# Kernel optimization log

Measured on AMD Instinct MI355X. Metric: run time of the kernel, lower is better.

The kernel has to match this reference:

```python
import jax, jax.numpy as jnp
import numpy as np


def _conv1x1(x, W, b):
    # x: (B, Ci, H, W), W: (Co, Ci), b: (Co,)
    return jnp.einsum('oi,bihw->bohw', W, x) + b[None, :, None, None]


def setup_inputs() -> dict:
    key = jax.random.key(0)
    ks = jax.random.split(key, 12)
    B, C, H, W = 4, 256, 64, 64
    d = C // 2
    prev_c = 512
    s = lambda k, shape, scale=0.05: (jax.random.normal(k, shape, dtype=jnp.float32) * scale)
    return {
        'source_enc_f': jax.random.normal(ks[0], (B, C, H, W), dtype=jnp.float32),
        'target_enc_f': jax.random.normal(ks[1], (B, C, H, W), dtype=jnp.float32),
        'prev_inp': jax.random.normal(ks[2], (B, prev_c, H // 2, W // 2), dtype=jnp.float32),
        'Wq': s(ks[3], (d, C)), 'bq': s(ks[4], (d,)),
        'Wk': s(ks[5], (d, C)), 'bk': s(ks[6], (d,)),
        'Wv': s(ks[7], (d, C)), 'bv': s(ks[8], (d,)),
        'Wp': s(ks[9], (C, d)), 'bp': s(ks[10], (C,)),
        'gamma': jnp.zeros((1,), dtype=jnp.float32) + 0.1,  # nonzero so attn path contributes
        'Wc': s(ks[11], (C, C + prev_c, 3, 3)),
        'bc': jnp.zeros((C,), dtype=jnp.float32),
    }


def reference(source_enc_f, target_enc_f, prev_inp, Wq, bq, Wk, bk, Wv, bv, Wp, bp, gamma, Wc, bc):
    B, C, H, W = source_enc_f.shape
    d = Wq.shape[0]
    HW = H * W

    # --- AttnMech ---
    q = _conv1x1(source_enc_f, Wq, bq)   # (B, d, H, W)
    k = _conv1x1(target_enc_f, Wk, bk)
    v = _conv1x1(target_enc_f, Wv, bv)

    kf = k.reshape(B, d, HW)             # (B, d, HW)
    qf = q.reshape(B, d, HW)             # (B, d, HW)
    # scores[b, i, j] = sum_c key[b, c, i] * query[b, c, j]; no 1/sqrt(d) scaling
    scores = jnp.einsum('bci,bcj->bij', kf, qf)       # (B, HW, HW)
    attn = jax.nn.softmax(scores, axis=1)             # softmax over key axis (torch dim=1)

    vf = v.transpose(0, 2, 3, 1).reshape(B, HW, d)    # (B, HW, d)
    out = jnp.einsum('bij,bjc->bic', attn, vf)        # (B, HW, d)
    out = out.reshape(B, H, W, d).transpose(0, 3, 1, 2)  # (B, d, H, W)
    out = _conv1x1(out, Wp, bp)                       # (B, C, H, W)
    x = target_enc_f + gamma[0] * out

    # --- upsample (nearest, scale 2) + concat ---
    prev = jnp.repeat(jnp.repeat(prev_inp, 2, axis=2), 2, axis=3)
    x = jnp.concatenate([x, prev], axis=1)            # (B, C+prev_c, H, W)

    # --- 3x3 conv, stride 1, pad 1 ---
    x = jax.lax.conv_general_dilated(
        x, Wc, window_strides=(1, 1), padding=((1, 1), (1, 1)),
        dimension_numbers=('NCHW', 'OIHW', 'NCHW'))
    x = x + bc[None, :, None, None]

    # --- InstanceNorm2d (affine=False, eps=1e-5, biased var over HW) ---
    mean = jnp.mean(x, axis=(2, 3), keepdims=True)
    var = jnp.mean(jnp.square(x - mean), axis=(2, 3), keepdims=True)
    x = (x - mean) * jax.lax.rsqrt(var + 1e-5)

    return jax.nn.relu(x)
```

## Files before the change

### kernel.cpp

```cpp
#include <hip/hip_runtime.h>
#include <hip/hip_bf16.h>

#define BB 4
#define CC 256
#define HW 4096
#define DD 128

typedef __attribute__((ext_vector_type(8))) short bf16x8;
typedef __attribute__((ext_vector_type(4))) short bf16x4;
typedef __attribute__((ext_vector_type(4))) float f32x4;
typedef __attribute__((ext_vector_type(16))) float f32x16;
typedef __attribute__((ext_vector_type(4))) unsigned uint4v;

static __device__ __forceinline__ void ld4(float* dst, const float* src) {
  float4 t = *(const float4*)src;
  dst[0] = t.x; dst[1] = t.y; dst[2] = t.z; dst[3] = t.w;
}

static __device__ __forceinline__ short f2b(float f) {
  unsigned u = __float_as_uint(f);
  u += 0x7fffu + ((u >> 16) & 1u);
  return (short)(u >> 16);
}
static __device__ __forceinline__ unsigned pk2(float lo, float hi) {
  return (unsigned)(unsigned short)f2b(lo) | ((unsigned)(unsigned short)f2b(hi) << 16);
}

static __device__ __forceinline__ void gl16(const short* g, short* l) {
  __builtin_amdgcn_global_load_lds(
      (const __attribute__((address_space(1))) unsigned*)g,
      (__attribute__((address_space(3))) unsigned*)l, 16, 0, 0);
}

__global__ __launch_bounds__(256) void k_qkv_mfma(
    const float* __restrict__ src, const float* __restrict__ tgt,
    const float* __restrict__ Wq, const float* __restrict__ bq,
    const float* __restrict__ Wk, const float* __restrict__ bk,
    const float* __restrict__ Wv, const float* __restrict__ bv,
    short* __restrict__ qb, short* __restrict__ kb, short* __restrict__ vb)
{
  __shared__ __align__(16) short Wt[128 * 40];
  __shared__ __align__(16) short Xt[64 * 40];
  __shared__ __align__(16) short T[9216];
  const int tid = threadIdx.x;
  const int wv = tid >> 6;
  const int lane = tid & 63;
  const int t = lane & 15, q = lane >> 4;
  const int px0 = blockIdx.x * 64;
  const int which = blockIdx.y;
  const int b = blockIdx.z;
  const float* X    = (which == 0) ? src : tgt;
  const float* Wm   = (which == 0) ? Wq : (which == 1) ? Wk : Wv;
  const float* bias = (which == 0) ? bq : (which == 1) ? bk : bv;

  const f32x4 zf = {0.f, 0.f, 0.f, 0.f};
  f32x4 acc[2][4];
#pragma unroll
  for (int mt = 0; mt < 2; ++mt)
#pragma unroll
    for (int nt = 0; nt < 4; ++nt) acc[mt][nt] = zf;

  for (int kk = 0; kk < CC; kk += 32) {
    __syncthreads();
#pragma unroll
    for (int u = 0; u < 4; ++u) {
      int e = tid + (u << 8);
      int row = e >> 3, cq = (e & 7) * 4;
      float4 w4 = *(const float4*)&Wm[row * CC + kk + cq];
      unsigned* dst = (unsigned*)(Wt + row * 40 + cq);
      dst[0] = pk2(w4.x, w4.y);
      dst[1] = pk2(w4.z, w4.w);
    }
#pragma unroll
    for (int u = 0; u < 2; ++u) {
      int e = tid + (u << 8);
      int c = e >> 4, p4 = (e & 15) * 4;
      float4 xv = *(const float4*)&X[((size_t)b * CC + kk + c) * HW + px0 + p4];
      Xt[(p4 + 0) * 40 + c] = f2b(xv.x);
      Xt[(p4 + 1) * 40 + c] = f2b(xv.y);
      Xt[(p4 + 2) * 40 + c] = f2b(xv.z);
      Xt[(p4 + 3) * 40 + c] = f2b(xv.w);
    }
    __syncthreads();
    bf16x8 af[2], bfr[4];
#pragma unroll
    for (int mt = 0; mt < 2; ++mt)
      af[mt] = *(const bf16x8*)(Wt + (wv * 32 + mt * 16 + t) * 40 + q * 8);
#pragma unroll
    for (int nt = 0; nt < 4; ++nt)
      bfr[nt] = *(const bf16x8*)(Xt + (nt * 16 + t) * 40 + q * 8);
#pragma unroll
    for (int mt = 0; mt < 2; ++mt)
#pragma unroll
      for (int nt = 0; nt < 4; ++nt)
        acc[mt][nt] = __builtin_amdgcn_mfma_f32_16x16x32_bf16(
            af[mt], bfr[nt], acc[mt][nt], 0, 0, 0);
  }
  __syncthreads();
  if (which < 2) {
#pragma unroll
    for (int mt = 0; mt < 2; ++mt) {
      int chb = wv * 32 + mt * 16 + q * 4;
#pragma unroll
      for (int r = 0; r < 4; ++r) {
        float bv_ = bias[chb + r];
#pragma unroll
        for (int nt = 0; nt < 4; ++nt)
          T[(nt * 16 + t) * 136 + chb + r] = f2b(acc[mt][nt][r] + bv_);
      }
    }
    __syncthreads();
    short* out = (which == 0) ? qb : kb;
    int p = tid >> 2, cq = (tid & 3) * 32;
    short* gdst = out + ((size_t)b * HW + px0 + p) * DD + cq;
#pragma unroll
    for (int e2 = 0; e2 < 4; ++e2)
      *(uint4*)(gdst + e2 * 8) = *(const uint4*)(T + p * 136 + cq + e2 * 8);
  } else {
#pragma unroll
    for (int mt = 0; mt < 2; ++mt) {
      int chb = wv * 32 + mt * 16 + q * 4;
#pragma unroll
      for (int r = 0; r < 4; ++r) {
        float bv_ = bias[chb + r];
#pragma unroll
        for (int nt = 0; nt < 4; ++nt)
          T[(chb + r) * 72 + nt * 16 + t] = f2b(acc[mt][nt][r] + bv_);
      }
    }
    __syncthreads();
    int ch = tid >> 1, pq = (tid & 1) * 32;
    short* gdst = vb + ((size_t)b * DD + ch) * HW + px0 + pq;
#pragma unroll
    for (int e2 = 0; e2 < 4; ++e2)
      *(uint4*)(gdst + e2 * 8) = *(const uint4*)(T + ch * 72 + pq + e2 * 8);
  }
}

__global__ __launch_bounds__(256) void k_lsum2(
    const short* __restrict__ qb, const short* __restrict__ kb,
    float* __restrict__ rl)
{
  __shared__ float lred[4][64];
  const int tid = threadIdx.x;
  const int w = tid >> 6;
  const int lane = tid & 63;
  const int t = lane & 15, q = lane >> 4;
  const int j0 = blockIdx.x * 64;
  const int ibeg = blockIdx.y * 1024;
  const int b = blockIdx.z;
  const short* qbb = qb + (size_t)b * HW * DD;
  const short* kbb = kb + (size_t)b * HW * DD;

  bf16x8 Bq[4][4];
#pragma unroll
  for (int nt = 0; nt < 4; ++nt)
#pragma unroll
    for (int kk = 0; kk < 4; ++kk)
      Bq[nt][kk] = *(const bf16x8*)(qbb + (size_t)(j0 + nt * 16 + t) * DD + kk * 32 + q * 8);

  float racc[4] = {0.f, 0.f, 0.f, 0.f};
  const f32x4 zf = {0.f, 0.f, 0.f, 0.f};

  for (int i = ibeg + w * 16; i < ibeg + 1024; i += 64) {
    bf16x8 Ak[4];
#pragma unroll
    for (int kk = 0; kk < 4; ++kk)
      Ak[kk] = *(const bf16x8*)(kbb + (size_t)(i + t) * DD + kk * 32 + q * 8);
#pragma unroll
    for (int nt = 0; nt < 4; ++nt) {
      f32x4 d = zf;
#pragma unroll
      for (int kk = 0; kk < 4; ++kk)
        d = __builtin_amdgcn_mfma_f32_16x16x32_bf16(Ak[kk], Bq[nt][kk], d, 0, 0, 0);
      racc[nt] += __expf(d[0]) + __expf(d[1]) + __expf(d[2]) + __expf(d[3]);
    }
  }
#pragma unroll
  for (int nt = 0; nt < 4; ++nt) {
    float r = racc[nt];
    r += __shfl_xor(r, 16);
    r += __shfl_xor(r, 32);
    if (q == 0) lred[w][nt * 16 + t] = r;
  }
  __syncthreads();
  if (tid < 64) {
    float sum = lred[0][tid] + lred[1][tid] + lred[2][tid] + lred[3][tid];
    atomicAdd(&rl[(size_t)b * HW + j0 + tid], sum);
  }
}

__global__ __launch_bounds__(256) void k_vs(
    const short* __restrict__ vb, const float* __restrict__ rl,
    short* __restrict__ vs)
{
  int id4 = (blockIdx.x * 256 + threadIdx.x) * 4;
  int j = id4 & (HW - 1);
  int b = id4 >> 19;
  uint2 pv = *(const uint2*)(vb + id4);
  float f0 = __uint_as_float(pv.x << 16);
  float f1 = __uint_as_float(pv.x & 0xffff0000u);
  float f2 = __uint_as_float(pv.y << 16);
  float f3 = __uint_as_float(pv.y & 0xffff0000u);
  const float* rlb = rl + (size_t)b * HW + j;
  unsigned u0 = pk2(f0 / rlb[0], f1 / rlb[1]);
  unsigned u1 = pk2(f2 / rlb[2], f3 / rlb[3]);
  *(uint2*)(vs + id4) = make_uint2(u0, u1);
}

__global__ __launch_bounds__(256, 2) void k_attn2(
    const short* __restrict__ qb, const short* __restrict__ kb,
    const short* __restrict__ vs, float* __restrict__ ao)
{
  __shared__ __align__(16) short Qs[2][64 * 128];
  __shared__ __align__(16) short Vp[2][128 * 72];
  const int tid = threadIdx.x;
  const int w = tid >> 6;
  const int lane = tid & 63;
  const int l31 = lane & 31, h = lane >> 5;
  const int b = blockIdx.z;
  const int i0w = blockIdx.x * 128 + w * 32;
  const int jbeg = blockIdx.y * 1024, jend = jbeg + 1024;
  const short* qbb = qb + (size_t)b * HW * DD;
  const short* kbb = kb + (size_t)b * HW * DD;
  const short* vsb = vs + (size_t)b * DD * HW;

  bf16x8 Bk[8];
#pragma unroll
  for (int kk = 0; kk < 8; ++kk)
    Bk[kk] = *(const bf16x8*)(kbb + (size_t)(i0w + l31) * DD + kk * 16 + h * 8);

  f32x16 acc[4];
#pragma unroll
  for (int nt = 0; nt < 4; ++nt)
#pragma unroll
    for (int e = 0; e < 16; ++e) acc[nt][e] = 0.f;

  bf16x8 rq[4], rv[4];
#define LOADT(jt)                                                             \
  {                                                                           \
    _Pragma("unroll")                                                         \
    for (int r = 0; r < 4; ++r) {                                             \
      int e = tid + (r << 8);                                                 \
      rq[r] = *(const bf16x8*)(qbb + (size_t)((jt) + (e >> 4)) * DD +         \
                               (e & 15) * 8);                                 \
      rv[r] = *(const bf16x8*)(vsb + (size_t)(e >> 3) * HW + (jt) +           \
                               (e & 7) * 8);                                  \
    }                                                                         \
  }
#define WRITET(buf)                                                           \
  {                                                                           \
    _Pragma("unroll")                                                         \
    for (int r = 0; r < 4; ++r) {                                             \
      int e = tid + (r << 8);                                                 \
      int row = e >> 4;                                                       \
      int slot = (e & 15) ^ (row & 15);                                       \
      *(bf16x8*)(Qs[buf] + row * 128 + slot * 8) = rq[r];                     \
    }                                                                         \
    _Pragma("unroll")                                                         \
    for (int r = 0; r < 4; ++r) {                                             \
      int e = tid + (r << 8);                                                 \
      int c = e >> 3, u8 = e & 7;                                             \
      int kap = (u8 >> 2) * 32 + ((u8 >> 1) & 1) * 16 + (u8 & 1) * 4;         \
      bf16x4 lo = __builtin_shufflevector(rv[r], rv[r], 0, 1, 2, 3);          \
      bf16x4 hi = __builtin_shufflevector(rv[r], rv[r], 4, 5, 6, 7);          \
      *(bf16x4*)(Vp[buf] + c * 72 + kap) = lo;                                \
      *(bf16x4*)(Vp[buf] + c * 72 + kap + 8) = hi;                            \
    }                                                                         \
  }

  LOADT(jbeg);
  WRITET(0);
  LOADT(jbeg + 64);

  int cur = 0;
  for (int j = jbeg; j < jend; j += 64) {
    __syncthreads();
    if (j + 64 < jend) {
      WRITET(cur ^ 1);
      if (j + 128 < jend) LOADT(j + 128);
    }
    const short* Qb = Qs[cur];
    const short* Vb = Vp[cur];
    f32x16 sv[2];
#pragma unroll
    for (int ntj = 0; ntj < 2; ++ntj)
#pragma unroll
      for (int e = 0; e < 16; ++e) sv[ntj][e] = 0.f;
#pragma unroll
    for (int ntj = 0; ntj < 2; ++ntj)
#pragma unroll
      for (int kk = 0; kk < 8; ++kk) {
        int row = ntj * 32 + l31;
        int slot = (kk * 2 + h) ^ (row & 15);
        bf16x8 aq = *(const bf16x8*)(Qb + row * 128 + slot * 8);
        sv[ntj] = __builtin_amdgcn_mfma_f32_32x32x16_bf16(aq, Bk[kk], sv[ntj], 0, 0, 0);
      }
    bf16x8 ap[4];
#pragma unroll
    for (int s = 0; s < 4; ++s) {
      const int tI = s >> 1, base = (s & 1) * 8;
      unsigned w0 = pk2(__expf(sv[tI][base + 0]), __expf(sv[tI][base + 1]));
      unsigned w1 = pk2(__expf(sv[tI][base + 2]), __expf(sv[tI][base + 3]));
      unsigned w2 = pk2(__expf(sv[tI][base + 4]), __expf(sv[tI][base + 5]));
      unsigned w3 = pk2(__expf(sv[tI][base + 6]), __expf(sv[tI][base + 7]));
      uint4v pw = {w0, w1, w2, w3};
      ap[s] = __builtin_bit_cast(bf16x8, pw);
    }
#pragma unroll
    for (int ntc = 0; ntc < 4; ++ntc)
#pragma unroll
      for (int s = 0; s < 4; ++s) {
        bf16x8 bv = *(const bf16x8*)(Vb + (ntc * 32 + l31) * 72 + s * 16 + h * 8);
        acc[ntc] = __builtin_amdgcn_mfma_f32_32x32x16_bf16(ap[s], bv, acc[ntc], 0, 0, 0);
      }
    cur ^= 1;
  }
#undef LOADT
#undef WRITET
  float* aob = ao + (size_t)b * HW * DD;
#pragma unroll
  for (int ntc = 0; ntc < 4; ++ntc)
#pragma unroll
    for (int rg = 0; rg < 16; ++rg) {
      int i = i0w + (rg & 3) + 8 * (rg >> 2) + 4 * h;
      atomicAdd(&aob[(size_t)i * DD + ntc * 32 + l31], acc[ntc][rg]);
    }
}

__global__ __launch_bounds__(256) void k_proj(
    const float* __restrict__ ao, const float* __restrict__ tgt,
    const float* __restrict__ Wp, const float* __restrict__ bp,
    const float* __restrict__ gamma, short* __restrict__ Xn)
{
  __shared__ float Wt[32][132];
  __shared__ float Xs[32][68];
  __shared__ float T[64][133];
  const int tid = threadIdx.x;
  const int tx = tid & 15, ty = tid >> 4;
  const int p0 = blockIdx.x * 64;
  const int ro = blockIdx.y * 128;
  const int b = blockIdx.z;
  const float g0 = gamma[0];

  float acc[8][4];
#pragma unroll
  for (int i = 0; i < 8; ++i)
#pragma unroll
    for (int j = 0; j < 4; ++j) acc[i][j] = 0.f;

  for (int kk = 0; kk < DD; kk += 32) {
    __syncthreads();
#pragma unroll
    for (int u = 0; u < 4; ++u) {
      int e = tid + 256 * u;
      int c4 = (e & 7) * 4, r = e >> 3;
      float w[4]; ld4(w, &Wp[(ro + r) * DD + kk + c4]);
      Wt[c4 + 0][r] = w[0]; Wt[c4 + 1][r] = w[1];
      Wt[c4 + 2][r] = w[2]; Wt[c4 + 3][r] = w[3];
    }
#pragma unroll
    for (int u = 0; u < 2; ++u) {
      int e = tid + 256 * u;
      int p = e >> 3, c4 = (e & 7) * 4;
      float4 v = *(const float4*)&ao[((size_t)b * HW + p0 + p) * DD + kk + c4];
      Xs[c4 + 0][p] = v.x; Xs[c4 + 1][p] = v.y;
      Xs[c4 + 2][p] = v.z; Xs[c4 + 3][p] = v.w;
    }
    __syncthreads();
#pragma unroll 4
    for (int c = 0; c < 32; ++c) {
      float wa[8], xb[4];
      ld4(wa, &Wt[c][ty * 8]); ld4(wa + 4, &Wt[c][ty * 8 + 4]);
      ld4(xb, &Xs[c][tx * 4]);
#pragma unroll
      for (int rr = 0; rr < 8; ++rr)
#pragma unroll
        for (int pp = 0; pp < 4; ++pp) acc[rr][pp] += wa[rr] * xb[pp];
    }
  }
#pragma unroll
  for (int rr = 0; rr < 8; ++rr) {
    int r = ro + ty * 8 + rr;
    int idx = (b * CC + r) * HW + p0 + tx * 4;
    float4 t4 = *(const float4*)&tgt[idx];
    float bpv = bp[r];
    T[tx * 4 + 0][ty * 8 + rr] = t4.x + g0 * (acc[rr][0] + bpv);
    T[tx * 4 + 1][ty * 8 + rr] = t4.y + g0 * (acc[rr][1] + bpv);
    T[tx * 4 + 2][ty * 8 + rr] = t4.z + g0 * (acc[rr][2] + bpv);
    T[tx * 4 + 3][ty * 8 + rr] = t4.w + g0 * (acc[rr][3] + bpv);
  }
  __syncthreads();
  {
    int p = tid >> 2, cq = (tid & 3) * 32;
    int hh = p0 >> 6;
    unsigned* dst = (unsigned*)(Xn + ((((size_t)b * 66 + hh + 1) * 66) + 1 + p) * 768 + ro + cq);
#pragma unroll
    for (int e = 0; e < 16; ++e)
      dst[e] = pk2(T[p][cq + 2 * e], T[p][cq + 2 * e + 1]);
  }
}

__global__ __launch_bounds__(256) void k_pack(
    const float* __restrict__ prev, short* __restrict__ Xn)
{
  __shared__ float tile[64][65];
  const int tid = threadIdx.x;
  const int h = blockIdx.x;
  const int ci0 = blockIdx.y * 64;
  const int b = blockIdx.z;

  {
    int w = tid & 63, r = tid >> 6;
    for (int cs = r; cs < 64; cs += 4)
      tile[cs][w] = prev[((size_t)b * 512 + ci0 + cs) * 1024 + (h >> 1) * 32 + (w >> 1)];
  }
  __syncthreads();
  {
    int ci = tid & 63, wq = tid >> 6;
    for (int ws2 = wq; ws2 < 64; ws2 += 4)
      Xn[((((size_t)b * 66 + h + 1) * 66) + 1 + ws2) * 768 + 256 + ci0 + ci] = f2b(tile[ci][ws2]);
  }
}

__global__ __launch_bounds__(256) void k_wb(
    const float* __restrict__ Wc, short* __restrict__ Wb)
{
  int i = blockIdx.x * 256 + threadIdx.x;
  int o = i / 6912;
  int rem = i - o * 6912;
  int khw = rem / 768;
  int ci = rem - khw * 768;
  Wb[i] = f2b(Wc[(size_t)o * 6912 + ci * 9 + khw]);
}

__global__ __launch_bounds__(256, 2) void k_conv_mfma(
    const short* __restrict__ Xn,
    const short* __restrict__ Wb,
    float* __restrict__ outf,
    short* __restrict__ cb1)
{
  __shared__ __align__(16) short Wl[384 * 64];
  __shared__ __align__(16) short Xl[132 * 64];
  const int tid = threadIdx.x;
  const int wv = tid >> 6;
  const int lane = tid & 63;
  const int t = lane & 15, q = lane >> 4;
  const int wm = wv >> 1, wn = wv & 1;
  const int h0 = blockIdx.x * 2;
  const int m0 = (blockIdx.y >> 1) * 128;
  const int ks = blockIdx.y & 1;
  const int b = blockIdx.z;

  const f32x4 zf = {0.f, 0.f, 0.f, 0.f};
  f32x4 acc[4][4];
#pragma unroll
  for (int mt = 0; mt < 4; ++mt)
#pragma unroll
    for (int nt = 0; nt < 4; ++nt) acc[mt][nt] = zf;

  for (int kh = 0; kh < 3; ++kh) {
    const short* wsrc = Wb + (size_t)m0 * 6912 + (kh * 3) * 768 + ks * 384;
    const short* xsrc = Xn + ((size_t)b * 66 + h0 + kh) * 66 * 768 + ks * 384;
    for (int c6 = 0; c6 < 6; ++c6) {
      int ci0 = c6 * 64;
#pragma unroll
      for (int r = 0; r < 12; ++r) {
        int e = tid + (r << 8);
        int g = e & 7, row = e >> 3;
        int kw = row >> 7, cl = row & 127;
        int gs = g ^ (row & 7);
        gl16(wsrc + (size_t)cl * 6912 + kw * 768 + ci0 + gs * 8, Wl + e * 8);
      }
#pragma unroll
      for (int r = 0; r < 5; ++r) {
        int e = tid + (r << 8);
        if (e < 1056) {
          int g = e & 7, prow = e >> 3;
          int xrow = (prow * 993) >> 16;
          int px = prow - xrow * 66;
          int gs = g ^ (prow & 7);
          gl16(xsrc + ((size_t)xrow * 66 + px) * 768 + ci0 + gs * 8, Xl + e * 8);
        }
      }
      __syncthreads();
#pragma unroll
      for (int kw = 0; kw < 3; ++kw) {
        bf16x8 af[4][2], bfr[4][2];
#pragma unroll
        for (int kk = 0; kk < 2; ++kk) {
#pragma unroll
          for (int mt = 0; mt < 4; ++mt) {
            int row = kw * 128 + wm * 64 + mt * 16 + t;
            int g = (kk * 4 + q) ^ (row & 7);
            af[mt][kk] = *(const bf16x8*)(Wl + row * 64 + g * 8);
          }
#pragma unroll
          for (int nt = 0; nt < 4; ++nt) {
            int prow = wn * 66 + nt * 16 + t + kw;
            int g = (kk * 4 + q) ^ (prow & 7);
            bfr[nt][kk] = *(const bf16x8*)(Xl + prow * 64 + g * 8);
          }
        }
#pragma unroll
        for (int kk = 0; kk < 2; ++kk)
#pragma unroll
          for (int mt = 0; mt < 4; ++mt)
#pragma unroll
            for (int nt = 0; nt < 4; ++nt)
              acc[mt][nt] = __builtin_amdgcn_mfma_f32_16x16x32_bf16(
                  af[mt][kk], bfr[nt][kk], acc[mt][nt], 0, 0, 0);
      }
      __syncthreads();
    }
  }
  const int orow = h0 + wn;
  if (ks == 0) {
#pragma unroll
    for (int mt = 0; mt < 4; ++mt) {
      int om = m0 + wm * 64 + mt * 16 + q * 4;
#pragma unroll
      for (int r = 0; r < 4; ++r) {
        float* dst = outf + ((size_t)b * CC + om + r) * HW + orow * 64;
#pragma unroll
        for (int nt = 0; nt < 4; ++nt)
          dst[nt * 16 + t] = acc[mt][nt][r];
      }
    }
  } else {
#pragma unroll
    for (int mt = 0; mt < 4; ++mt) {
      int om = m0 + wm * 64 + mt * 16 + q * 4;
#pragma unroll
      for (int r = 0; r < 4; ++r) {
        short* dst = cb1 + ((size_t)b * CC + om + r) * HW + orow * 64;
#pragma unroll
        for (int nt = 0; nt < 4; ++nt)
          dst[nt * 16 + t] = f2b(acc[mt][nt][r]);
      }
    }
  }
}

__global__ __launch_bounds__(256) void k_inorm(
    const float* p0, const short* __restrict__ p1, float* out)
{
  __shared__ float buf[4096];
  __shared__ float red[8];
  const int tid = threadIdx.x;
  const int ch = blockIdx.x;
  const float* s0 = p0 + (size_t)ch * HW;
  const short* s1 = p1 + (size_t)ch * HW;

  float s = 0.f, sq = 0.f;
#pragma unroll
  for (int u = 0; u < 4; ++u) {
    int idx = u * 1024 + tid * 4;
    float4 a = *(const float4*)&s0[idx];
    uint2 pb = *(const uint2*)&s1[idx];
    float v0 = a.x + __uint_as_float(pb.x << 16);
    float v1 = a.y + __uint_as_float(pb.x & 0xffff0000u);
    float v2 = a.z + __uint_as_float(pb.y << 16);
    float v3 = a.w + __uint_as_float(pb.y & 0xffff0000u);
    buf[idx + 0] = v0; buf[idx + 1] = v1;
    buf[idx + 2] = v2; buf[idx + 3] = v3;
    s += v0 + v1 + v2 + v3;
    sq += v0 * v0 + v1 * v1 + v2 * v2 + v3 * v3;
  }
#pragma unroll
  for (int m = 32; m >= 1; m >>= 1) {
    s  += __shfl_xor(s, m, 64);
    sq += __shfl_xor(sq, m, 64);
  }
  if ((tid & 63) == 0) { red[tid >> 6] = s; red[4 + (tid >> 6)] = sq; }
  __syncthreads();
  if (tid == 0) {
    float S = red[0] + red[1] + red[2] + red[3];
    float Q = red[4] + red[5] + red[6] + red[7];
    float mean = S * (1.f / HW);
    float var = Q * (1.f / HW) - mean * mean;
    red[0] = mean;
    red[1] = rsqrtf(var + 1e-5f);
  }
  __syncthreads();
  const float mean = red[0], rs = red[1];
#pragma unroll
  for (int u = 0; u < 4; ++u) {
    int idx = u * 1024 + tid * 4;
    float4 v = *(const float4*)&buf[idx];
    float4 o4 = make_float4(fmaxf((v.x - mean) * rs, 0.f),
                            fmaxf((v.y - mean) * rs, 0.f),
                            fmaxf((v.z - mean) * rs, 0.f),
                            fmaxf((v.w - mean) * rs, 0.f));
    *(float4*)&out[(size_t)ch * HW + idx] = o4;
  }
}

extern "C" void kernel_launch(void* const* d_in, const int* in_sizes, int n_in,
                              void* d_out, int out_size, void* d_ws, size_t ws_size,
                              hipStream_t stream) {
  const float* src  = (const float*)d_in[0];
  const float* tgt  = (const float*)d_in[1];
  const float* prev = (const float*)d_in[2];
  const float* Wq = (const float*)d_in[3];  const float* bq = (const float*)d_in[4];
  const float* Wk = (const float*)d_in[5];  const float* bk = (const float*)d_in[6];
  const float* Wv = (const float*)d_in[7];  const float* bv = (const float*)d_in[8];
  const float* Wp = (const float*)d_in[9];  const float* bp = (const float*)d_in[10];
  const float* gamma = (const float*)d_in[11];
  const float* Wc = (const float*)d_in[12];

  float* ws = (float*)d_ws;
  short* qb = (short*)ws;
  short* kb = (short*)(ws + 1048576);
  short* vb = (short*)(ws + 2097152);
  float* rl = ws + 3145728;
  short* vs = (short*)(ws + 3162112);
  short* Xn = (short*)ws;
  float* ao = ws + 6690816;
  short* Wb = (short*)(ws + 8787968);
  float* outf = (float*)d_out;
  short* cb1 = (short*)(ws + 6690816);

  k_qkv_mfma<<<dim3(64, 3, BB), 256, 0, stream>>>(src, tgt, Wq, bq, Wk, bk, Wv, bv, qb, kb, vb);
  hipMemsetAsync(rl, 0, (size_t)BB * HW * 4, stream);
  k_lsum2<<<dim3(64, 4, BB), 256, 0, stream>>>(qb, kb, rl);
  k_vs   <<<dim3(2048),      256, 0, stream>>>(vb, rl, vs);
  hipMemsetAsync(ao, 0, (size_t)2097152 * 4, stream);
  k_attn2<<<dim3(32, 4, BB), 256, 0, stream>>>(qb, kb, vs, ao);
  hipMemsetAsync(Xn, 0, (size_t)BB * 66 * 66 * 768 * 2, stream);
  k_proj <<<dim3(64, 2, BB), 256, 0, stream>>>(ao, tgt, Wp, bp, gamma, Xn);
  k_pack <<<dim3(64, 8, BB), 256, 0, stream>>>(prev, Xn);
  k_wb   <<<dim3(6912),      256, 0, stream>>>(Wc, Wb);
  k_conv_mfma<<<dim3(32, 4, BB), 256, 0, stream>>>(Xn, Wb, outf, cb1);
  k_inorm<<<dim3(1024),      256, 0, stream>>>(outf, cb1, (float*)d_out);
}
```

Before: 331.3 us.

## Replace attention split-K fp32 atomics with bf16 partial buffers reduced in projection

When the workspace is large enough, each j-split block of the attention kernel stores its partial output as bf16 into its own slice instead of doing fp32 atomicAdd into a shared buffer. The projection kernel then sums the four partial slices while loading its input tile. This removes the memset of the accumulation buffer and the atomic traffic, at the cost of bf16 rounding on the partials and more bytes read in the projection. The path is chosen at runtime from the workspace size, and the partial slices share workspace with buffers that are written later.

```diff
diff --git a/kernel.cpp b/kernel.cpp
--- a/kernel.cpp
+++ b/kernel.cpp
@@ -210,7 +210,8 @@
 
 __global__ __launch_bounds__(256, 2) void k_attn2(
     const short* __restrict__ qb, const short* __restrict__ kb,
-    const short* __restrict__ vs, float* __restrict__ ao)
+    const short* __restrict__ vs, float* __restrict__ ao,
+    short* __restrict__ aop, int mode)
 {
   __shared__ __align__(16) short Qs[2][64 * 128];
   __shared__ __align__(16) short Vp[2][128 * 72];
@@ -318,20 +319,32 @@
   }
 #undef LOADT
 #undef WRITET
-  float* aob = ao + (size_t)b * HW * DD;
-#pragma unroll
-  for (int ntc = 0; ntc < 4; ++ntc)
-#pragma unroll
-    for (int rg = 0; rg < 16; ++rg) {
-      int i = i0w + (rg & 3) + 8 * (rg >> 2) + 4 * h;
-      atomicAdd(&aob[(size_t)i * DD + ntc * 32 + l31], acc[ntc][rg]);
-    }
+  if (mode) {
+    short* pdst = aop + ((size_t)blockIdx.y * BB + b) * HW * DD;
+#pragma unroll
+    for (int ntc = 0; ntc < 4; ++ntc)
+#pragma unroll
+      for (int rg = 0; rg < 16; ++rg) {
+        int i = i0w + (rg & 3) + 8 * (rg >> 2) + 4 * h;
+        pdst[(size_t)i * DD + ntc * 32 + l31] = f2b(acc[ntc][rg]);
+      }
+  } else {
+    float* aob = ao + (size_t)b * HW * DD;
+#pragma unroll
+    for (int ntc = 0; ntc < 4; ++ntc)
+#pragma unroll
+      for (int rg = 0; rg < 16; ++rg) {
+        int i = i0w + (rg & 3) + 8 * (rg >> 2) + 4 * h;
+        atomicAdd(&aob[(size_t)i * DD + ntc * 32 + l31], acc[ntc][rg]);
+      }
+  }
 }
 
 __global__ __launch_bounds__(256) void k_proj(
-    const float* __restrict__ ao, const float* __restrict__ tgt,
+    const float* __restrict__ ao, const short* __restrict__ aop,
+    const float* __restrict__ tgt,
     const float* __restrict__ Wp, const float* __restrict__ bp,
-    const float* __restrict__ gamma, short* __restrict__ Xn)
+    const float* __restrict__ gamma, short* __restrict__ Xn, int mode)
 {
   __shared__ float Wt[32][132];
   __shared__ float Xs[32][68];
@@ -359,13 +372,33 @@
       Wt[c4 + 0][r] = w[0]; Wt[c4 + 1][r] = w[1];
       Wt[c4 + 2][r] = w[2]; Wt[c4 + 3][r] = w[3];
     }
-#pragma unroll
-    for (int u = 0; u < 2; ++u) {
-      int e = tid + 256 * u;
-      int p = e >> 3, c4 = (e & 7) * 4;
-      float4 v = *(const float4*)&ao[((size_t)b * HW + p0 + p) * DD + kk + c4];
-      Xs[c4 + 0][p] = v.x; Xs[c4 + 1][p] = v.y;
-      Xs[c4 + 2][p] = v.z; Xs[c4 + 3][p] = v.w;
+    if (mode) {
+#pragma unroll
+      for (int u = 0; u < 2; ++u) {
+        int e = tid + 256 * u;
+        int p = e >> 3, c4 = (e & 7) * 4;
+        size_t base = ((size_t)b * HW + p0 + p) * DD + kk + c4;
+        float v0 = 0.f, v1 = 0.f, v2 = 0.f, v3 = 0.f;
+#pragma unroll
+        for (int js = 0; js < 4; ++js) {
+          uint2 pb = *(const uint2*)&aop[(size_t)js * BB * HW * DD + base];
+          v0 += __uint_as_float(pb.x << 16);
+          v1 += __uint_as_float(pb.x & 0xffff0000u);
+          v2 += __uint_as_float(pb.y << 16);
+          v3 += __uint_as_float(pb.y & 0xffff0000u);
+        }
+        Xs[c4 + 0][p] = v0; Xs[c4 + 1][p] = v1;
+        Xs[c4 + 2][p] = v2; Xs[c4 + 3][p] = v3;
+      }
+    } else {
+#pragma unroll
+      for (int u = 0; u < 2; ++u) {
+        int e = tid + 256 * u;
+        int p = e >> 3, c4 = (e & 7) * 4;
+        float4 v = *(const float4*)&ao[((size_t)b * HW + p0 + p) * DD + kk + c4];
+        Xs[c4 + 0][p] = v.x; Xs[c4 + 1][p] = v.y;
+        Xs[c4 + 2][p] = v.z; Xs[c4 + 3][p] = v.w;
+      }
     }
     __syncthreads();
 #pragma unroll 4
@@ -620,15 +653,17 @@
   short* Wb = (short*)(ws + 8787968);
   float* outf = (float*)d_out;
   short* cb1 = (short*)(ws + 6690816);
+  short* aop = (short*)(ws + 6690816);
+  const int mode = (ws_size >= 43540480ull) ? 1 : 0;
 
   k_qkv_mfma<<<dim3(64, 3, BB), 256, 0, stream>>>(src, tgt, Wq, bq, Wk, bk, Wv, bv, qb, kb, vb);
   hipMemsetAsync(rl, 0, (size_t)BB * HW * 4, stream);
   k_lsum2<<<dim3(64, 4, BB), 256, 0, stream>>>(qb, kb, rl);
   k_vs   <<<dim3(2048),      256, 0, stream>>>(vb, rl, vs);
-  hipMemsetAsync(ao, 0, (size_t)2097152 * 4, stream);
-  k_attn2<<<dim3(32, 4, BB), 256, 0, stream>>>(qb, kb, vs, ao);
+  if (!mode) hipMemsetAsync(ao, 0, (size_t)2097152 * 4, stream);
+  k_attn2<<<dim3(32, 4, BB), 256, 0, stream>>>(qb, kb, vs, ao, aop, mode);
   hipMemsetAsync(Xn, 0, (size_t)BB * 66 * 66 * 768 * 2, stream);
-  k_proj <<<dim3(64, 2, BB), 256, 0, stream>>>(ao, tgt, Wp, bp, gamma, Xn);
+  k_proj <<<dim3(64, 2, BB), 256, 0, stream>>>(ao, aop, tgt, Wp, bp, gamma, Xn, mode);
   k_pack <<<dim3(64, 8, BB), 256, 0, stream>>>(prev, Xn);
   k_wb   <<<dim3(6912),      256, 0, stream>>>(Wc, Wb);
   k_conv_mfma<<<dim3(32, 4, BB), 256, 0, stream>>>(Xn, Wb, outf, cb1);
```

Result: faster. 317.0 us, median of 2 (-4.3%).
